# Optimization experiments

Hardware: AMD Instinct MI355X
Metric: run time of the kernel (lower is better)

Reference implementation:

```python
import jax, jax.numpy as jnp
import numpy as np

N = 500000   # nodes (total bases across sequences)
E = 2 * N    # edges, degree-2 sequence graph
F = 128      # filters
BN_EPS = 1e-3  # Keras BatchNormalization default epsilon


def setup_inputs() -> dict:
    key = jax.random.key(0)
    ks = jax.random.split(key, 10)
    x = jax.random.normal(ks[0], (N, F), jnp.float32)
    # segment ids: sorted, each node appears twice (tf.math.segment_sum requires sorted ids)
    seg = jnp.repeat(jnp.arange(N, dtype=jnp.int32), 2)
    pairs_prev = jnp.stack([seg, jax.random.randint(ks[1], (E,), 0, N, jnp.int32)], axis=1)
    pairs_next = jnp.stack([seg, jax.random.randint(ks[2], (E,), 0, N, jnp.int32)], axis=1)
    s = 0.05  # 'random_normal' initializer stddev
    wNext = jax.random.normal(ks[3], (F, F), jnp.float32) * s
    wPrev = jax.random.normal(ks[4], (F, F), jnp.float32) * s
    b = jnp.zeros((1, F), jnp.float32)
    # GRUCell(F): kernel [F,3F], recurrent_kernel [F,3F], bias [2,3F] (reset_after=True)
    gru_kernel = jax.random.normal(ks[5], (F, 3 * F), jnp.float32) * s
    gru_recurrent_kernel = jax.random.normal(ks[6], (F, 3 * F), jnp.float32) * s
    gru_bias = jnp.zeros((2, 3 * F), jnp.float32)
    bn_gamma = jnp.ones((F,), jnp.float32)
    bn_beta = jnp.zeros((F,), jnp.float32)
    bn_mean = jax.random.normal(ks[7], (F,), jnp.float32) * 0.05
    bn_var = jnp.ones((F,), jnp.float32) + jax.random.uniform(ks[8], (F,), jnp.float32) * 0.1
    return {"x": x, "pairs_prev": pairs_prev, "pairs_next": pairs_next,
            "wNext": wNext, "wPrev": wPrev, "b": b,
            "gru_kernel": gru_kernel, "gru_recurrent_kernel": gru_recurrent_kernel,
            "gru_bias": gru_bias, "bn_gamma": bn_gamma, "bn_beta": bn_beta,
            "bn_mean": bn_mean, "bn_var": bn_var}


def reference(x, pairs_prev, pairs_next, wNext, wPrev, b,
              gru_kernel, gru_recurrent_kernel, gru_bias,
              bn_gamma, bn_beta, bn_mean, bn_var):
    n = x.shape[0]
    # gather neighbor features + segment_sum aggregation
    prev_sumx = jax.ops.segment_sum(x[pairs_prev[:, 1]], pairs_prev[:, 0], num_segments=n)
    next_sumx = jax.ops.segment_sum(x[pairs_next[:, 1]], pairs_next[:, 0], num_segments=n)
    # aggre = next@Wn + prev@Wp + b ; non-padded, multiply=False -> + x
    aggre = next_sumx @ wNext + prev_sumx @ wPrev + b + x
    # activation then BatchNorm (inference mode, training=False)
    a = jax.nn.relu(aggre)
    a = bn_gamma * (a - bn_mean) * jax.lax.rsqrt(bn_var + BN_EPS) + bn_beta
    # GRUCell(F) update with state h = x (Keras reset_after=True)
    mx = a @ gru_kernel + gru_bias[0]        # [N, 3F]
    mh = x @ gru_recurrent_kernel + gru_bias[1]
    xz, xr, xh = jnp.split(mx, 3, axis=-1)
    rz, rr, rh = jnp.split(mh, 3, axis=-1)
    z = jax.nn.sigmoid(xz + rz)
    r = jax.nn.sigmoid(xr + rr)
    hh = jnp.tanh(xh + r * rh)
    return z * x + (1.0 - z) * hh
```

## Files before the change

### kernel.cpp

```cpp
#include <hip/hip_runtime.h>
#include <hip/hip_bf16.h>
#include <stdint.h>

#define FDIM 128
#define AS1 __attribute__((address_space(1)))
#define AS3 __attribute__((address_space(3)))

typedef short bf16x8 __attribute__((ext_vector_type(8)));
typedef float f32x4 __attribute__((ext_vector_type(4)));

__device__ __forceinline__ unsigned short f2bf(float f) {
    union { float f; unsigned int u; } v; v.f = f;
    unsigned int r = v.u + 0x7FFFu + ((v.u >> 16) & 1u);
    return (unsigned short)(r >> 16);
}
__device__ __forceinline__ unsigned int pack2bf(float a, float b) {
    return (unsigned int)f2bf(a) | ((unsigned int)f2bf(b) << 16);
}
__device__ __forceinline__ float bflo(unsigned int u) {
    union { unsigned int u; float f; } v; v.u = u << 16; return v.f;
}
__device__ __forceinline__ float bfhi(unsigned int u) {
    union { unsigned int u; float f; } v; v.u = u & 0xFFFF0000u; return v.f;
}
__device__ __forceinline__ float bf2f(unsigned short u) {
    union { unsigned int u; float f; } v; v.u = (unsigned int)u << 16; return v.f;
}
__device__ __forceinline__ unsigned int addpk(unsigned int a, unsigned int b) {
    float lo = bflo(a) + bflo(b);
    float hi = bfhi(a) + bfhi(b);
    unsigned int d;
    asm("v_cvt_pk_bf16_f32 %0, %1, %2" : "=v"(d) : "v"(lo), "v"(hi));
    return d;
}

__global__ void prep_kernel(const float* __restrict__ wNext, const float* __restrict__ wPrev,
                            const float* __restrict__ gk, const float* __restrict__ gr,
                            const float* __restrict__ gb, const float* __restrict__ gamma,
                            const float* __restrict__ beta, const float* __restrict__ mean,
                            const float* __restrict__ var,
                            unsigned short* __restrict__ bt1, unsigned short* __restrict__ bt2,
                            float* __restrict__ bias2, float* __restrict__ bnscale,
                            float* __restrict__ bnshift)
{
    int t = blockIdx.x * blockDim.x + threadIdx.x;
    if (t < 32768) {
        int n = t >> 8, k = t & 255;
        float v = (k < 128) ? wNext[k * 128 + n] : wPrev[(k - 128) * 128 + n];
        unsigned int byte = (unsigned)n * 512u + (((unsigned)(k * 2)) ^ (((unsigned)(n & 15)) << 4));
        *(unsigned short*)((unsigned char*)bt1 + byte) = f2bf(v);
    } else if (t < 32768 + 131072) {
        int e = t - 32768;
        int n = e >> 8, k = e & 255;
        float v;
        if (n < 256)      v = (k < 128) ? gk[k * 384 + n] : gr[(k - 128) * 384 + n];
        else if (n < 384) v = (k < 128) ? gk[k * 384 + n] : 0.f;
        else              v = (k < 128) ? 0.f : gr[(k - 128) * 384 + (n - 128)];
        int g = n >> 7, fl = n & 127;
        int nn = ((fl >> 4) << 6) + (g << 4) + (fl & 15);
        unsigned int byte = (unsigned)nn * 512u + (((unsigned)(k * 2)) ^ (((unsigned)(nn & 15)) << 4));
        *(unsigned short*)((unsigned char*)bt2 + byte) = f2bf(v);
    } else if (t < 32768 + 131072 + 512) {
        int n = t - (32768 + 131072);
        float v;
        if (n < 256)      v = gb[n] + gb[384 + n];
        else if (n < 384) v = gb[n];
        else              v = gb[384 + (n - 128)];
        bias2[n] = v;
    } else if (t < 32768 + 131072 + 512 + 128) {
        int f = t - (32768 + 131072 + 512);
        float s = gamma[f] * rsqrtf(var[f] + 1e-3f);
        bnscale[f] = s;
        bnshift[f] = beta[f] - mean[f] * s;
    }
}

__global__ __launch_bounds__(256) void x_convert(const float* __restrict__ x,
                                                 unsigned short* __restrict__ xbf, int Nn)
{
    const int total = Nn * 32;
    const float4* x4 = (const float4*)x;
    for (int t = blockIdx.x * 256 + threadIdx.x; t < total; t += gridDim.x * 256) {
        int m = t >> 5, l = t & 31;
        float4 v = x4[t];
        unsigned int lo = pack2bf(v.x, v.y), hi = pack2bf(v.z, v.w);
        unsigned int byte = (unsigned)m * 256u + (((unsigned)(l * 8)) ^ (((unsigned)(m & 15)) << 4));
        uint2 pk; pk.x = lo; pk.y = hi;
        *(uint2*)((unsigned char*)xbf + byte) = pk;
    }
}

__attribute__((amdgpu_waves_per_eu(4, 8)))
__global__ __launch_bounds__(512) void k_gather_g1(
    const unsigned short* __restrict__ xbf,
    const int* __restrict__ pprev, const int* __restrict__ pnext,
    const unsigned short* __restrict__ bt1,
    const float* __restrict__ bvec, const float* __restrict__ bnscale,
    const float* __restrict__ bnshift,
    unsigned short* __restrict__ a_out, int Nn)
{
    __shared__ __align__(16) unsigned char lds[49152];
    const int tid = threadIdx.x, wid = tid >> 6, lane = tid & 63;
    const int col0 = lane & 15, kq = lane >> 4;
    const unsigned int rs = (unsigned)col0 << 4;

    const unsigned char* bt1b = (const unsigned char*)bt1;
    bf16x8 b1[8];
#pragma unroll
    for (int kk = 0; kk < 8; kk++)
        b1[kk] = *(const bf16x8*)(bt1b + (unsigned)(wid * 16 + col0) * 512u +
                                  (((unsigned)(kk * 64 + kq * 16)) ^ rs));
#pragma unroll
    for (int kk = 0; kk < 8; kk++) asm volatile("" : "+v"(b1[kk]));

    const int f = wid * 16 + col0;
    const float bb = bvec[f], sc = bnscale[f], sh = bnshift[f];

    const int rg = tid >> 3, s8 = tid & 7, dirp = s8 >> 2, pg = s8 & 3;
    const int* pid = dirp ? pprev : pnext;
    const unsigned char* xb = (const unsigned char*)xbf;

    const int G = (int)gridDim.x;
    const int tiles = (Nn + 63) >> 6;

    uint4 g0[4], g1[4];
    int4 idxA = {0, 0, 0, 0}, idxB;
    { int gn = blockIdx.x * 64 + rg; if (gn < Nn) idxA = *(const int4*)(pid + (size_t)4 * gn); }

    for (int t = blockIdx.x; t < tiles; t += G) {
        const int base = t * 64;
        {
            size_t xg = (size_t)base * 256u + (unsigned)(wid * 2048) + (unsigned)(lane * 16);
            __builtin_amdgcn_global_load_lds((const AS1 unsigned int*)(xb + xg),
                (AS3 unsigned int*)(lds + 32768u + (unsigned)(wid * 2048)), 16, 0, 0);
            __builtin_amdgcn_global_load_lds((const AS1 unsigned int*)(xb + xg + 1024),
                (AS3 unsigned int*)(lds + 32768u + (unsigned)(wid * 2048) + 1024u), 16, 0, 0);
        }
        {
            int gi0 = idxA.y, gi1 = idxA.w;
            unsigned sw0 = ((unsigned)(gi0 & 15)) << 4, sw1 = ((unsigned)(gi1 & 15)) << 4;
            const unsigned char* r0 = xb + (size_t)gi0 * 256u;
            const unsigned char* r1 = xb + (size_t)gi1 * 256u;
#pragma unroll
            for (int j = 0; j < 4; j++) {
                unsigned off = (unsigned)(pg * 64 + j * 16);
                g0[j] = *(const uint4*)(r0 + (off ^ sw0));
                g1[j] = *(const uint4*)(r1 + (off ^ sw1));
            }
        }
        __builtin_amdgcn_sched_barrier(0);
        idxB = (int4){0, 0, 0, 0};
        {
            int gn = (t + G) * 64 + rg;
            if (t + G < tiles && gn < Nn) idxB = *(const int4*)(pid + (size_t)4 * gn);
        }
        __builtin_amdgcn_sched_barrier(0);
        asm volatile("s_waitcnt vmcnt(1)" ::: "memory");
        __builtin_amdgcn_sched_barrier(0);
        {
            unsigned char* Sd = lds + (unsigned)(rg * 512 + dirp * 256);
            unsigned swd = ((unsigned)(rg & 15)) << 4;
#pragma unroll
            for (int j = 0; j < 4; j++) {
                uint4 a = g0[j], b = g1[j], d;
                d.x = addpk(a.x, b.x); d.y = addpk(a.y, b.y);
                d.z = addpk(a.z, b.z); d.w = addpk(a.w, b.w);
                *(uint4*)(Sd + (((unsigned)(pg * 64 + j * 16)) ^ swd)) = d;
            }
        }
        asm volatile("s_waitcnt lgkmcnt(0)" ::: "memory");
        __builtin_amdgcn_sched_barrier(0);
        __builtin_amdgcn_s_barrier();

        f32x4 acc1[4];
#pragma unroll
        for (int m = 0; m < 4; m++) acc1[m] = (f32x4){bb, bb, bb, bb};
#pragma unroll
        for (int kk = 0; kk < 8; kk++) {
            unsigned ko = ((unsigned)(kk * 64 + kq * 16)) ^ rs;
            bf16x8 a0 = *(const bf16x8*)(lds + (unsigned)(0 * 16 + col0) * 512u + ko);
            bf16x8 a1 = *(const bf16x8*)(lds + (unsigned)(1 * 16 + col0) * 512u + ko);
            bf16x8 a2 = *(const bf16x8*)(lds + (unsigned)(2 * 16 + col0) * 512u + ko);
            bf16x8 a3 = *(const bf16x8*)(lds + (unsigned)(3 * 16 + col0) * 512u + ko);
            acc1[0] = __builtin_amdgcn_mfma_f32_16x16x32_bf16(a0, b1[kk], acc1[0], 0, 0, 0);
            acc1[1] = __builtin_amdgcn_mfma_f32_16x16x32_bf16(a1, b1[kk], acc1[1], 0, 0, 0);
            acc1[2] = __builtin_amdgcn_mfma_f32_16x16x32_bf16(a2, b1[kk], acc1[2], 0, 0, 0);
            acc1[3] = __builtin_amdgcn_mfma_f32_16x16x32_bf16(a3, b1[kk], acc1[3], 0, 0, 0);
        }
        {
            const unsigned char* X = lds + 32768u;
#pragma unroll
            for (int m = 0; m < 4; m++) {
#pragma unroll
                for (int i = 0; i < 4; i++) {
                    int r = m * 16 + kq * 4 + i;
                    int grow = base + r;
                    if (grow < Nn) {
                        unsigned sw = ((unsigned)(r & 15)) << 4;
                        unsigned co = ((unsigned)(f * 2)) ^ sw;
                        float xv = bf2f(*(const unsigned short*)(X + (unsigned)r * 256u + co));
                        float v = acc1[m][i] + xv;
                        v = fmaxf(v, 0.f) * sc + sh;
                        __builtin_nontemporal_store(
                            f2bf(v),
                            (unsigned short*)((unsigned char*)a_out + (size_t)grow * 256u + co));
                    }
                }
            }
        }
        __builtin_amdgcn_s_barrier();
        idxA = idxB;
    }
}

__attribute__((amdgpu_waves_per_eu(2, 2)))
__global__ __launch_bounds__(512) void k_g2_gru(
    const unsigned short* __restrict__ a_in, const unsigned short* __restrict__ xbf,
    const unsigned short* __restrict__ bt2p, const float* __restrict__ bias2,
    float* __restrict__ out, int Nn)
{
    __shared__ __align__(16) unsigned char lds[65536];
    const int tid = threadIdx.x, wid = tid >> 6, lane = tid & 63;
    const int col0 = lane & 15, kq = lane >> 4;
    const unsigned int rs = (unsigned)col0 << 4;

    const unsigned char* bt2b = (const unsigned char*)bt2p;
    bf16x8 b2z[8], b2r[8], b2xh[4], b2rh[4];
#pragma unroll
    for (int kk = 0; kk < 8; kk++) {
        b2z[kk] = *(const bf16x8*)(bt2b + (unsigned)(wid * 64 + 0 + col0) * 512u + (((unsigned)(kk * 64 + kq * 16)) ^ rs));
        b2r[kk] = *(const bf16x8*)(bt2b + (unsigned)(wid * 64 + 16 + col0) * 512u + (((unsigned)(kk * 64 + kq * 16)) ^ rs));
    }
#pragma unroll
    for (int kk = 0; kk < 4; kk++) {
        b2xh[kk] = *(const bf16x8*)(bt2b + (unsigned)(wid * 64 + 32 + col0) * 512u + (((unsigned)(kk * 64 + kq * 16)) ^ rs));
        b2rh[kk] = *(const bf16x8*)(bt2b + (unsigned)(wid * 64 + 48 + col0) * 512u + (((unsigned)((kk + 4) * 64 + kq * 16)) ^ rs));
    }
#pragma unroll
    for (int kk = 0; kk < 8; kk++) {
        asm volatile("" : "+v"(b2z[kk]));
        asm volatile("" : "+v"(b2r[kk]));
    }
#pragma unroll
    for (int kk = 0; kk < 4; kk++) {
        asm volatile("" : "+v"(b2xh[kk]));
        asm volatile("" : "+v"(b2rh[kk]));
    }

    const int f = wid * 16 + col0;
    const float cz = bias2[f], cr = bias2[128 + f], cxh = bias2[256 + f], crh = bias2[384 + f];

    const unsigned char* aB = (const unsigned char*)a_in;
    const unsigned char* xB = (const unsigned char*)xbf;
    const int G = (int)gridDim.x;
    const int tiles = (Nn + 63) >> 6;

#define STAGE2(tt, pp) do {                                                                  \
    size_t g_ = (size_t)(tt) * 16384u + (unsigned)(wid * 2048) + (unsigned)(lane * 16);      \
    unsigned o_ = (unsigned)(pp) * 32768u + (unsigned)(wid * 2048);                          \
    __builtin_amdgcn_global_load_lds((const AS1 unsigned int*)(aB + g_),                     \
                                     (AS3 unsigned int*)(lds + o_), 16, 0, 0);               \
    __builtin_amdgcn_global_load_lds((const AS1 unsigned int*)(aB + g_ + 1024),              \
                                     (AS3 unsigned int*)(lds + o_ + 1024), 16, 0, 0);        \
    __builtin_amdgcn_global_load_lds((const AS1 unsigned int*)(xB + g_),                     \
                                     (AS3 unsigned int*)(lds + o_ + 16384u), 16, 0, 0);      \
    __builtin_amdgcn_global_load_lds((const AS1 unsigned int*)(xB + g_ + 1024),              \
                                     (AS3 unsigned int*)(lds + o_ + 16384u + 1024), 16, 0, 0);\
} while (0)

    STAGE2(blockIdx.x, 0);
    asm volatile("s_waitcnt vmcnt(0)" ::: "memory");
    __builtin_amdgcn_sched_barrier(0);
    __builtin_amdgcn_s_barrier();

    int p = 0;
    for (int t = blockIdx.x; t < tiles; t += G) {
        const int base = t * 64;
        {
            int tn = t + G;
            int tc = (tn < tiles) ? tn : t;
            STAGE2(tc, p ^ 1);
        }
        const unsigned char* A_ = lds + (unsigned)p * 32768u;
        const unsigned char* X_ = lds + (unsigned)p * 32768u + 16384u;

#pragma unroll
        for (int half = 0; half < 2; half++) {
            f32x4 az[2], ar[2], axh[2], arh[2];
#pragma unroll
            for (int mm = 0; mm < 2; mm++) {
                az[mm]  = (f32x4){cz, cz, cz, cz};
                ar[mm]  = (f32x4){cr, cr, cr, cr};
                axh[mm] = (f32x4){cxh, cxh, cxh, cxh};
                arh[mm] = (f32x4){crh, crh, crh, crh};
            }
#pragma unroll
            for (int kk = 0; kk < 8; kk++) {
                bf16x8 a2f[2];
#pragma unroll
                for (int mm = 0; mm < 2; mm++) {
                    int m = half * 2 + mm;
                    if (kk < 4)
                        a2f[mm] = *(const bf16x8*)(A_ + (unsigned)(m * 16 + col0) * 256u +
                                                   (((unsigned)(kk * 64 + kq * 16)) ^ rs));
                    else
                        a2f[mm] = *(const bf16x8*)(X_ + (unsigned)(m * 16 + col0) * 256u +
                                                   (((unsigned)((kk - 4) * 64 + kq * 16)) ^ rs));
                }
#pragma unroll
                for (int mm = 0; mm < 2; mm++) {
                    az[mm] = __builtin_amdgcn_mfma_f32_16x16x32_bf16(a2f[mm], b2z[kk], az[mm], 0, 0, 0);
                    ar[mm] = __builtin_amdgcn_mfma_f32_16x16x32_bf16(a2f[mm], b2r[kk], ar[mm], 0, 0, 0);
                    if (kk < 4)
                        axh[mm] = __builtin_amdgcn_mfma_f32_16x16x32_bf16(a2f[mm], b2xh[kk], axh[mm], 0, 0, 0);
                    else
                        arh[mm] = __builtin_amdgcn_mfma_f32_16x16x32_bf16(a2f[mm], b2rh[kk - 4], arh[mm], 0, 0, 0);
                }
            }
#pragma unroll
            for (int mm = 0; mm < 2; mm++) {
                int m = half * 2 + mm;
#pragma unroll
                for (int i = 0; i < 4; i++) {
                    int r = m * 16 + kq * 4 + i;
                    int grow = base + r;
                    if (grow < Nn) {
                        float z  = __builtin_amdgcn_rcpf(1.f + __expf(-az[mm][i]));
                        float rr = __builtin_amdgcn_rcpf(1.f + __expf(-ar[mm][i]));
                        float u  = axh[mm][i] + rr * arh[mm][i];
                        float th = 1.f - 2.f * __builtin_amdgcn_rcpf(__expf(2.f * u) + 1.f);
                        unsigned sw = ((unsigned)(r & 15)) << 4;
                        float xv = bf2f(*(const unsigned short*)(X_ + (unsigned)r * 256u +
                                                                 (((unsigned)(f * 2)) ^ sw)));
                        __builtin_nontemporal_store(th + z * (xv - th),
                                                    out + (size_t)grow * FDIM + f);
                    }
                }
            }
        }
        asm volatile("s_waitcnt vmcnt(16) lgkmcnt(0)" ::: "memory");
        __builtin_amdgcn_sched_barrier(0);
        __builtin_amdgcn_s_barrier();
        p ^= 1;
    }
#undef STAGE2
}

extern "C" void kernel_launch(void* const* d_in, const int* in_sizes, int n_in,
                              void* d_out, int out_size, void* d_ws, size_t ws_size,
                              hipStream_t stream)
{
    const float* x      = (const float*)d_in[0];
    const int*   pprev  = (const int*)d_in[1];
    const int*   pnext  = (const int*)d_in[2];
    const float* wNext  = (const float*)d_in[3];
    const float* wPrev  = (const float*)d_in[4];
    const float* b      = (const float*)d_in[5];
    const float* gk     = (const float*)d_in[6];
    const float* gr     = (const float*)d_in[7];
    const float* gb     = (const float*)d_in[8];
    const float* gamma  = (const float*)d_in[9];
    const float* beta   = (const float*)d_in[10];
    const float* mean   = (const float*)d_in[11];
    const float* var    = (const float*)d_in[12];
    float* out = (float*)d_out;
    const int Nn = in_sizes[0] / FDIM;

    unsigned char* ws = (unsigned char*)d_ws;
    unsigned short* xbf  = (unsigned short*)(ws + 0);
    unsigned short* a_ws = (unsigned short*)(ws + (size_t)Nn * 256u);
    size_t off_bt = (size_t)Nn * 512u;
    unsigned short* bt1   = (unsigned short*)(ws + off_bt);
    unsigned short* bt2   = (unsigned short*)(ws + off_bt + 65536);
    float* bias2          = (float*)(ws + off_bt + 327680);
    float* bnscale        = (float*)(ws + off_bt + 327680 + 2048);
    float* bnshift        = (float*)(ws + off_bt + 327680 + 2048 + 512);

    prep_kernel<<<643, 256, 0, stream>>>(wNext, wPrev, gk, gr, gb, gamma, beta, mean, var,
                                         bt1, bt2, bias2, bnscale, bnshift);
    x_convert<<<2048, 256, 0, stream>>>(x, xbf, Nn);
    k_gather_g1<<<512, 512, 0, stream>>>(xbf, pprev, pnext, bt1, b, bnscale, bnshift, a_ws, Nn);
    k_g2_gru<<<256, 512, 0, stream>>>(a_ws, xbf, bt2, bias2, out, Nn);
}
```

Measured before the change: 378.9 us.

## Gather neighbor rows from an fp8 copy of x to halve gather bytes

```diff
diff --git a/kernel.cpp b/kernel.cpp
--- a/kernel.cpp
+++ b/kernel.cpp
@@ -8,6 +8,7 @@
 
 typedef short bf16x8 __attribute__((ext_vector_type(8)));
 typedef float f32x4 __attribute__((ext_vector_type(4)));
+typedef float f32x2 __attribute__((ext_vector_type(2)));
 
 __device__ __forceinline__ unsigned short f2bf(float f) {
     union { float f; unsigned int u; } v; v.f = f;
@@ -17,21 +18,20 @@
 __device__ __forceinline__ unsigned int pack2bf(float a, float b) {
     return (unsigned int)f2bf(a) | ((unsigned int)f2bf(b) << 16);
 }
-__device__ __forceinline__ float bflo(unsigned int u) {
-    union { unsigned int u; float f; } v; v.u = u << 16; return v.f;
-}
-__device__ __forceinline__ float bfhi(unsigned int u) {
-    union { unsigned int u; float f; } v; v.u = u & 0xFFFF0000u; return v.f;
-}
 __device__ __forceinline__ float bf2f(unsigned short u) {
     union { unsigned int u; float f; } v; v.u = (unsigned int)u << 16; return v.f;
 }
-__device__ __forceinline__ unsigned int addpk(unsigned int a, unsigned int b) {
-    float lo = bflo(a) + bflo(b);
-    float hi = bfhi(a) + bfhi(b);
-    unsigned int d;
-    asm("v_cvt_pk_bf16_f32 %0, %1, %2" : "=v"(d) : "v"(lo), "v"(hi));
-    return d;
+__device__ __forceinline__ uint2 sum4fp8(unsigned int w0, unsigned int w1) {
+    f32x2 a0 = __builtin_amdgcn_cvt_pk_f32_fp8((int)w0, false);
+    f32x2 a1 = __builtin_amdgcn_cvt_pk_f32_fp8((int)w0, true);
+    f32x2 b0 = __builtin_amdgcn_cvt_pk_f32_fp8((int)w1, false);
+    f32x2 b1 = __builtin_amdgcn_cvt_pk_f32_fp8((int)w1, true);
+    float s0 = a0.x + b0.x, s1 = a0.y + b0.y;
+    float s2 = a1.x + b1.x, s3 = a1.y + b1.y;
+    uint2 r;
+    asm("v_cvt_pk_bf16_f32 %0, %1, %2" : "=v"(r.x) : "v"(s0), "v"(s1));
+    asm("v_cvt_pk_bf16_f32 %0, %1, %2" : "=v"(r.y) : "v"(s2), "v"(s3));
+    return r;
 }
 
 __global__ void prep_kernel(const float* __restrict__ wNext, const float* __restrict__ wPrev,
@@ -76,23 +76,32 @@
 }
 
 __global__ __launch_bounds__(256) void x_convert(const float* __restrict__ x,
-                                                 unsigned short* __restrict__ xbf, int Nn)
-{
-    const int total = Nn * 32;
+                                                 unsigned short* __restrict__ xbf,
+                                                 unsigned char* __restrict__ xq, int Nn)
+{
+    const int total = Nn * 16;
     const float4* x4 = (const float4*)x;
     for (int t = blockIdx.x * 256 + threadIdx.x; t < total; t += gridDim.x * 256) {
-        int m = t >> 5, l = t & 31;
-        float4 v = x4[t];
-        unsigned int lo = pack2bf(v.x, v.y), hi = pack2bf(v.z, v.w);
-        unsigned int byte = (unsigned)m * 256u + (((unsigned)(l * 8)) ^ (((unsigned)(m & 15)) << 4));
-        uint2 pk; pk.x = lo; pk.y = hi;
-        *(uint2*)((unsigned char*)xbf + byte) = pk;
+        int m = t >> 4, l = t & 15;
+        float4 v0 = x4[m * 32 + l * 2];
+        float4 v1 = x4[m * 32 + l * 2 + 1];
+        uint4 pk;
+        pk.x = pack2bf(v0.x, v0.y); pk.y = pack2bf(v0.z, v0.w);
+        pk.z = pack2bf(v1.x, v1.y); pk.w = pack2bf(v1.z, v1.w);
+        unsigned int byte = (unsigned)m * 256u + (((unsigned)(l * 16)) ^ (((unsigned)(m & 15)) << 4));
+        *(uint4*)((unsigned char*)xbf + byte) = pk;
+        int q0 = __builtin_amdgcn_cvt_pk_fp8_f32(v0.x, v0.y, 0, false);
+        q0 = __builtin_amdgcn_cvt_pk_fp8_f32(v0.z, v0.w, q0, true);
+        int q1 = __builtin_amdgcn_cvt_pk_fp8_f32(v1.x, v1.y, 0, false);
+        q1 = __builtin_amdgcn_cvt_pk_fp8_f32(v1.z, v1.w, q1, true);
+        uint2 qq; qq.x = (unsigned)q0; qq.y = (unsigned)q1;
+        *(uint2*)(xq + (size_t)m * 128u + (unsigned)(l * 8)) = qq;
     }
 }
 
 __attribute__((amdgpu_waves_per_eu(4, 8)))
 __global__ __launch_bounds__(512) void k_gather_g1(
-    const unsigned short* __restrict__ xbf,
+    const unsigned short* __restrict__ xbf, const unsigned char* __restrict__ xq,
     const int* __restrict__ pprev, const int* __restrict__ pnext,
     const unsigned short* __restrict__ bt1,
     const float* __restrict__ bvec, const float* __restrict__ bnscale,
@@ -123,7 +132,7 @@
     const int G = (int)gridDim.x;
     const int tiles = (Nn + 63) >> 6;
 
-    uint4 g0[4], g1[4];
+    uint4 q0a, q0b, q1a, q1b;
     int4 idxA = {0, 0, 0, 0}, idxB;
     { int gn = blockIdx.x * 64 + rg; if (gn < Nn) idxA = *(const int4*)(pid + (size_t)4 * gn); }
 
@@ -137,16 +146,12 @@
                 (AS3 unsigned int*)(lds + 32768u + (unsigned)(wid * 2048) + 1024u), 16, 0, 0);
         }
         {
-            int gi0 = idxA.y, gi1 = idxA.w;
-            unsigned sw0 = ((unsigned)(gi0 & 15)) << 4, sw1 = ((unsigned)(gi1 & 15)) << 4;
-            const unsigned char* r0 = xb + (size_t)gi0 * 256u;
-            const unsigned char* r1 = xb + (size_t)gi1 * 256u;
-#pragma unroll
-            for (int j = 0; j < 4; j++) {
-                unsigned off = (unsigned)(pg * 64 + j * 16);
-                g0[j] = *(const uint4*)(r0 + (off ^ sw0));
-                g1[j] = *(const uint4*)(r1 + (off ^ sw1));
-            }
+            const unsigned char* r0 = xq + (size_t)idxA.y * 128u + (unsigned)(pg * 32);
+            const unsigned char* r1 = xq + (size_t)idxA.w * 128u + (unsigned)(pg * 32);
+            q0a = *(const uint4*)(r0);
+            q0b = *(const uint4*)(r0 + 16);
+            q1a = *(const uint4*)(r1);
+            q1b = *(const uint4*)(r1 + 16);
         }
         __builtin_amdgcn_sched_barrier(0);
         idxB = (int4){0, 0, 0, 0};
@@ -160,13 +165,20 @@
         {
             unsigned char* Sd = lds + (unsigned)(rg * 512 + dirp * 256);
             unsigned swd = ((unsigned)(rg & 15)) << 4;
-#pragma unroll
-            for (int j = 0; j < 4; j++) {
-                uint4 a = g0[j], b = g1[j], d;
-                d.x = addpk(a.x, b.x); d.y = addpk(a.y, b.y);
-                d.z = addpk(a.z, b.z); d.w = addpk(a.w, b.w);
-                *(uint4*)(Sd + (((unsigned)(pg * 64 + j * 16)) ^ swd)) = d;
-            }
+            uint2 e0, e1;
+            uint4 d;
+            e0 = sum4fp8(q0a.x, q1a.x); e1 = sum4fp8(q0a.y, q1a.y);
+            d.x = e0.x; d.y = e0.y; d.z = e1.x; d.w = e1.y;
+            *(uint4*)(Sd + (((unsigned)(pg * 64 + 0)) ^ swd)) = d;
+            e0 = sum4fp8(q0a.z, q1a.z); e1 = sum4fp8(q0a.w, q1a.w);
+            d.x = e0.x; d.y = e0.y; d.z = e1.x; d.w = e1.y;
+            *(uint4*)(Sd + (((unsigned)(pg * 64 + 16)) ^ swd)) = d;
+            e0 = sum4fp8(q0b.x, q1b.x); e1 = sum4fp8(q0b.y, q1b.y);
+            d.x = e0.x; d.y = e0.y; d.z = e1.x; d.w = e1.y;
+            *(uint4*)(Sd + (((unsigned)(pg * 64 + 32)) ^ swd)) = d;
+            e0 = sum4fp8(q0b.z, q1b.z); e1 = sum4fp8(q0b.w, q1b.w);
+            d.x = e0.x; d.y = e0.y; d.z = e1.x; d.w = e1.y;
+            *(uint4*)(Sd + (((unsigned)(pg * 64 + 48)) ^ swd)) = d;
         }
         asm volatile("s_waitcnt lgkmcnt(0)" ::: "memory");
         __builtin_amdgcn_sched_barrier(0);
@@ -369,7 +381,8 @@
     unsigned char* ws = (unsigned char*)d_ws;
     unsigned short* xbf  = (unsigned short*)(ws + 0);
     unsigned short* a_ws = (unsigned short*)(ws + (size_t)Nn * 256u);
-    size_t off_bt = (size_t)Nn * 512u;
+    unsigned char*  xq   = (unsigned char*)(ws + (size_t)Nn * 512u);
+    size_t off_bt = (size_t)Nn * 640u;
     unsigned short* bt1   = (unsigned short*)(ws + off_bt);
     unsigned short* bt2   = (unsigned short*)(ws + off_bt + 65536);
     float* bias2          = (float*)(ws + off_bt + 327680);
@@ -378,7 +391,7 @@
 
     prep_kernel<<<643, 256, 0, stream>>>(wNext, wPrev, gk, gr, gb, gamma, beta, mean, var,
                                          bt1, bt2, bias2, bnscale, bnshift);
-    x_convert<<<2048, 256, 0, stream>>>(x, xbf, Nn);
-    k_gather_g1<<<512, 512, 0, stream>>>(xbf, pprev, pnext, bt1, b, bnscale, bnshift, a_ws, Nn);
+    x_convert<<<2048, 256, 0, stream>>>(x, xbf, xq, Nn);
+    k_gather_g1<<<768, 512, 0, stream>>>(xbf, xq, pprev, pnext, bt1, b, bnscale, bnshift, a_ws, Nn);
     k_g2_gru<<<256, 512, 0, stream>>>(a_ws, xbf, bt2, bias2, out, Nn);
 }
```

Measured after the change: 330.1 us, median of 2. 1.15x faster.
